# Performance work log

Measured on AMD Instinct MI355X. Metric: run time of the kernel, lower is better.

## Reference

```python
import jax, jax.numpy as jnp
import numpy as np

N = 50000
E = 800000
IN_CH, CDK, EDGE_DIM = 40, 200, 10
HID, HEADS = 64, 4
NEG_SLOPE = 0.2
SM_EPS = 1e-16
BN_EPS = 1e-5


def _glorot(key, shape):
    fan = shape[0] + shape[-1]
    return jax.random.normal(key, shape, jnp.float32) * jnp.sqrt(2.0 / fan)


def setup_inputs() -> dict:
    key = jax.random.key(0)
    ks = iter(jax.random.split(key, 40))
    inp = {
        'x': jax.random.normal(next(ks), (N, IN_CH), jnp.float32),
        'cdk_desc': jax.random.normal(next(ks), (N, CDK), jnp.float32),
        'edge_src': jax.random.randint(next(ks), (E,), 0, N, jnp.int32),
        'edge_dst': jax.random.randint(next(ks), (E,), 0, N, jnp.int32),
        'edge_attr': jax.random.normal(next(ks), (E, EDGE_DIM), jnp.float32),
    }
    dims = [(IN_CH + CDK, HEADS, HID), (HID * HEADS, HEADS, HID), (HID * HEADS, 1, HID)]
    for i, (din, h, c) in enumerate(dims):
        inp[f'W{i}'] = _glorot(next(ks), (din, h * c))
        inp[f'as{i}'] = _glorot(next(ks), (h, c))
        inp[f'ad{i}'] = _glorot(next(ks), (h, c))
        inp[f'We{i}'] = _glorot(next(ks), (EDGE_DIM, h * c))
        inp[f'ae{i}'] = _glorot(next(ks), (h, c))
        inp[f'b{i}'] = jnp.zeros((h * c,), jnp.float32)
        inp[f'g{i}'] = jnp.ones((h * c,), jnp.float32)
        inp[f'be{i}'] = jnp.zeros((h * c,), jnp.float32)
    inp['linW'] = _glorot(next(ks), (HID, 1))
    inp['linB'] = jnp.zeros((1,), jnp.float32)
    return inp


def gat_conv(x, src, dst, ea, W, a_s, a_d, We, a_e, b, heads, c):
    # PyG GATConv: shared linear for src/dst, edge features, segment softmax.
    xp = (x @ W).reshape(N, heads, c)                 # [N,H,C]
    ep = (ea @ We).reshape(-1, heads, c)              # [Etot,H,C]
    al_s = (xp * a_s).sum(-1)                         # [N,H]
    al_d = (xp * a_d).sum(-1)                         # [N,H]
    al_e = (ep * a_e).sum(-1)                         # [Etot,H]
    alpha = jax.nn.leaky_relu(al_s[src] + al_d[dst] + al_e, NEG_SLOPE)
    m = jax.ops.segment_max(alpha, dst, num_segments=N)
    ex = jnp.exp(alpha - m[dst])
    den = jax.ops.segment_sum(ex, dst, num_segments=N)
    att = ex / (den[dst] + SM_EPS)                    # [Etot,H]
    out = jax.ops.segment_sum(xp[src] * att[:, :, None], dst, num_segments=N)
    return out.reshape(N, heads * c) + b


def batch_norm(x, g, be):
    mu = x.mean(0)
    var = x.var(0)
    return g * (x - mu) * jax.lax.rsqrt(var + BN_EPS) + be


def reference(x, cdk_desc, edge_src, edge_dst, edge_attr,
              W0, as0, ad0, We0, ae0, b0, g0, be0,
              W1, as1, ad1, We1, ae1, b1, g1, be1,
              W2, as2, ad2, We2, ae2, b2, g2, be2,
              linW, linB):
    # add self-loops once (PyG default add_self_loops=True, fill_value='mean')
    loop = jnp.arange(N, dtype=edge_src.dtype)
    src = jnp.concatenate([edge_src, loop])
    dst = jnp.concatenate([edge_dst, loop])
    ea_mean = edge_attr.mean(0)
    ea = jnp.concatenate([edge_attr, jnp.broadcast_to(ea_mean, (N, EDGE_DIM))], 0)

    h = jnp.concatenate([x, cdk_desc], axis=-1)
    layers = [
        (W0, as0, ad0, We0, ae0, b0, g0, be0, HEADS),
        (W1, as1, ad1, We1, ae1, b1, g1, be1, HEADS),
        (W2, as2, ad2, We2, ae2, b2, g2, be2, 1),
    ]
    for (W, a_s, a_d, We, a_e, b, g, be, heads) in layers:
        h = gat_conv(h, src, dst, ea, W, a_s, a_d, We, a_e, b, heads, HID)
        h = batch_norm(h, g, be)
        h = jax.nn.elu(h)
        # dropout is identity in eval mode
    out = h @ linW + linB
    return jax.nn.sigmoid(out).squeeze(-1)
```

## Files before the change

### kernel.cpp

```cpp
#include <hip/hip_runtime.h>
#include <math.h>

#define NNODES 50000
#define NEDGES 800000
#define ETOT   (NNODES + NEDGES)
#define EDIM   10
#define SMEPS  1e-16f
#define BNEPS  1e-5f
#define NSLOPE 0.2f

#define SCANB  ((NNODES + 255) / 256)
#define EASUMB 256
#define BNB    256

typedef _Float16 f16;
typedef f16 f16x8 __attribute__((ext_vector_type(8)));
typedef f16 f16x4 __attribute__((ext_vector_type(4)));
typedef float f32x4 __attribute__((ext_vector_type(4)));


__global__ void k_deg(const int* __restrict__ edst, int* __restrict__ deg) {
    int e = blockIdx.x * blockDim.x + threadIdx.x;
    if (e >= ETOT) return;
    int d = (e < NEDGES) ? edst[e] : (e - NEDGES);
    atomicAdd(&deg[d], 1);
}

__global__ void k_easum(const float* __restrict__ ea, float* __restrict__ part) {
    float acc[EDIM];
#pragma unroll
    for (int d = 0; d < EDIM; ++d) acc[d] = 0.f;
    int tid = blockIdx.x * blockDim.x + threadIdx.x;
    const int np = NEDGES / 2;
    for (int p = tid; p < np; p += gridDim.x * blockDim.x) {
        const float4* q = (const float4*)&ea[(long)p * 20];
        float4 v0 = q[0], v1 = q[1], v2 = q[2], v3 = q[3], v4 = q[4];
        acc[0] += v0.x + v2.z;
        acc[1] += v0.y + v2.w;
        acc[2] += v0.z + v3.x;
        acc[3] += v0.w + v3.y;
        acc[4] += v1.x + v3.z;
        acc[5] += v1.y + v3.w;
        acc[6] += v1.z + v4.x;
        acc[7] += v1.w + v4.y;
        acc[8] += v2.x + v4.z;
        acc[9] += v2.y + v4.w;
    }
    __shared__ float sm[256];
    for (int d = 0; d < EDIM; ++d) {
        sm[threadIdx.x] = acc[d];
        __syncthreads();
        for (int s = 128; s > 0; s >>= 1) {
            if (threadIdx.x < s) sm[threadIdx.x] += sm[threadIdx.x + s];
            __syncthreads();
        }
        if (threadIdx.x == 0) part[blockIdx.x * EDIM + d] = sm[0];
        __syncthreads();
    }
}

__global__ void k_scan1(const int* __restrict__ deg, int* __restrict__ off,
                        int* __restrict__ partials) {
    __shared__ int sm[256];
    int t = threadIdx.x;
    int i = blockIdx.x * 256 + t;
    int v = (i < NNODES) ? deg[i] : 0;
    sm[t] = v;
    __syncthreads();
    int val = v;
    for (int d = 1; d < 256; d <<= 1) {
        int tv = (t >= d) ? sm[t - d] : 0;
        __syncthreads();
        val += tv;
        sm[t] = val;
        __syncthreads();
    }
    if (i < NNODES) off[i] = val - v;
    if (t == 255) partials[blockIdx.x] = val;
}

__global__ void k_scan2(int* __restrict__ partials, int* __restrict__ off) {
    __shared__ int sm[256];
    int t = threadIdx.x;
    int v = (t < SCANB) ? partials[t] : 0;
    sm[t] = v;
    __syncthreads();
    int val = v;
    for (int d = 1; d < 256; d <<= 1) {
        int tv = (t >= d) ? sm[t - d] : 0;
        __syncthreads();
        val += tv;
        sm[t] = val;
        __syncthreads();
    }
    if (t < SCANB) partials[t] = val - v;
    if (t == 255) off[NNODES] = ETOT;
}

__global__ void k_scan3(int* __restrict__ off, const int* __restrict__ partials) {
    int i = blockIdx.x * 256 + threadIdx.x;
    if (i < NNODES) off[i] += partials[blockIdx.x];
}

__global__ void k_scatter(const int* __restrict__ esrc, const int* __restrict__ edst,
                          const int* __restrict__ off, int* __restrict__ cursor,
                          int* __restrict__ csr_src, int* __restrict__ perm) {
    int e = blockIdx.x * blockDim.x + threadIdx.x;
    if (e >= ETOT) return;
    int s, d;
    if (e < NEDGES) { s = esrc[e]; d = edst[e]; }
    else            { s = d = e - NEDGES; }
    int pos  = atomicAdd(&cursor[d], 1);
    int slot = off[d] + pos;
    csr_src[slot] = s;
    perm[e] = slot;
}

__global__ void k_concat_h(const float* __restrict__ x, const float* __restrict__ cdk,
                           f16* __restrict__ out) {
    int i = blockIdx.x * blockDim.x + threadIdx.x;
    if (i >= NNODES * 256) return;
    int n = i >> 8, j = i & 255;
    float v = (j < 40) ? x[n * 40 + j] : (j < 240) ? cdk[n * 200 + (j - 40)] : 0.f;
    out[i] = (f16)v;
}

__global__ void k_wcvt_all(const float* __restrict__ W0, const float* __restrict__ W1,
                           const float* __restrict__ W2, f16* __restrict__ Wt0,
                           f16* __restrict__ Wt1, f16* __restrict__ Wt2) {
    int i = blockIdx.x * blockDim.x + threadIdx.x;
    const float* W; f16* Wt; int K, NC, j;
    if (i < 65536)       { W = W0; Wt = Wt0; K = 240; NC = 256; j = i; }
    else if (i < 131072) { W = W1; Wt = Wt1; K = 256; NC = 256; j = i - 65536; }
    else if (i < 147456) { W = W2; Wt = Wt2; K = 256; NC = 64;  j = i - 131072; }
    else return;
    int n = j >> 8, k = j & 255;
    Wt[j] = (k < K) ? (f16)W[k * NC + n] : (f16)0.f;
}

#define GM_LDS 40
__global__ __launch_bounds__(256) void k_gemm_h(const f16* __restrict__ A,
                                                const f16* __restrict__ Bt,
                                                f16* __restrict__ C,
                                                int M, int NC) {
    __shared__ f16 As[128 * GM_LDS];
    __shared__ f16 Bs[64 * GM_LDS];
    const int t    = threadIdx.x;
    const int w    = t >> 6;
    const int lane = t & 63;
    const int row0 = blockIdx.x * 128;
    const int col0 = blockIdx.y * 64;

    const int ar = t >> 1;
    const int ak = (t & 1) * 16;
    const int bn = t >> 2;
    const int bk = (t & 3) * 8;

    const int l16 = lane & 15;
    const int kg  = lane >> 4;

    f32x4 acc[2][4];
#pragma unroll
    for (int i = 0; i < 2; ++i)
#pragma unroll
        for (int j = 0; j < 4; ++j) acc[i][j] = {0.f, 0.f, 0.f, 0.f};

    for (int k0 = 0; k0 < 256; k0 += 32) {
        f16x8 av0, av1;
#pragma unroll
        for (int i = 0; i < 8; ++i) { av0[i] = (f16)0.f; av1[i] = (f16)0.f; }
        if (row0 + ar < M) {
            const f16* ap = &A[(long)(row0 + ar) * 256 + k0 + ak];
            av0 = *(const f16x8*)ap;
            av1 = *(const f16x8*)(ap + 8);
        }
        *(f16x8*)&As[ar * GM_LDS + ak]     = av0;
        *(f16x8*)&As[ar * GM_LDS + ak + 8] = av1;
        f16x8 bv = *(const f16x8*)&Bt[(long)(col0 + bn) * 256 + k0 + bk];
        *(f16x8*)&Bs[bn * GM_LDS + bk] = bv;
        __syncthreads();

        f16x8 afr[2], bfr[4];
#pragma unroll
        for (int mi = 0; mi < 2; ++mi)
            afr[mi] = *(const f16x8*)&As[(w * 32 + mi * 16 + l16) * GM_LDS + kg * 8];
#pragma unroll
        for (int ni = 0; ni < 4; ++ni)
            bfr[ni] = *(const f16x8*)&Bs[(ni * 16 + l16) * GM_LDS + kg * 8];
#pragma unroll
        for (int mi = 0; mi < 2; ++mi)
#pragma unroll
            for (int ni = 0; ni < 4; ++ni)
                acc[mi][ni] = __builtin_amdgcn_mfma_f32_16x16x32_f16(
                    afr[mi], bfr[ni], acc[mi][ni], 0, 0, 0);
        __syncthreads();
    }
#pragma unroll
    for (int mi = 0; mi < 2; ++mi)
#pragma unroll
        for (int ni = 0; ni < 4; ++ni)
#pragma unroll
            for (int j = 0; j < 4; ++j) {
                int r = row0 + w * 32 + mi * 16 + kg * 4 + j;
                if (r < M) C[(long)r * NC + col0 + ni * 16 + l16] = (f16)acc[mi][ni][j];
            }
}

template <int H>
__global__ __launch_bounds__(256) void k_attn_node(const f16* __restrict__ xp,
                                                   const float* __restrict__ a_s,
                                                   const float* __restrict__ a_d,
                                                   float* __restrict__ als,
                                                   float* __restrict__ ald) {
    int gw   = (blockIdx.x * blockDim.x + threadIdx.x) >> 6;
    int lane = threadIdx.x & 63;
    if (gw >= NNODES) return;
    if constexpr (H == 4) {
        int h = lane >> 4, c4 = (lane & 15) * 4;
        f16x4 xh = *(const f16x4*)&xp[(long)gw * 256 + lane * 4];
        float4 xv = make_float4((float)xh[0], (float)xh[1], (float)xh[2], (float)xh[3]);
        float4 ws = *(const float4*)&a_s[h * 64 + c4];
        float4 wd = *(const float4*)&a_d[h * 64 + c4];
        float ps = xv.x * ws.x + xv.y * ws.y + xv.z * ws.z + xv.w * ws.w;
        float pd = xv.x * wd.x + xv.y * wd.y + xv.z * wd.z + xv.w * wd.w;
        for (int o = 1; o < 16; o <<= 1) { ps += __shfl_xor(ps, o); pd += __shfl_xor(pd, o); }
        if ((lane & 15) == 0) { als[gw * 4 + h] = ps; ald[gw * 4 + h] = pd; }
    } else {
        float xv = (float)xp[(long)gw * 64 + lane];
        float ps = xv * a_s[lane];
        float pd = xv * a_d[lane];
        for (int o = 1; o < 64; o <<= 1) { ps += __shfl_xor(ps, o); pd += __shfl_xor(pd, o); }
        if (lane == 0) { als[gw] = ps; ald[gw] = pd; }
    }
}

__global__ void k_ve_all(const float* __restrict__ We0, const float* __restrict__ ae0,
                         const float* __restrict__ We1, const float* __restrict__ ae1,
                         const float* __restrict__ We2, const float* __restrict__ ae2,
                         const float* __restrict__ eapart,
                         float* __restrict__ VeAll, float* __restrict__ laAll) {
    int l = blockIdx.x;
    const float* We = (l == 0) ? We0 : (l == 1) ? We1 : We2;
    const float* ae = (l == 0) ? ae0 : (l == 1) ? ae1 : ae2;
    int H = (l == 2) ? 1 : 4;
    float* Ve = VeAll + l * 48;
    float* la = laAll + l * 4;
    int t = threadIdx.x;

    float ac[EDIM];
#pragma unroll
    for (int d = 0; d < EDIM; ++d) ac[d] = 0.f;
    for (int r = t; r < EASUMB; r += 64) {
#pragma unroll
        for (int d = 0; d < EDIM; ++d) ac[d] += eapart[r * EDIM + d];
    }
#pragma unroll
    for (int o = 1; o < 64; o <<= 1) {
#pragma unroll
        for (int d = 0; d < EDIM; ++d) ac[d] += __shfl_xor(ac[d], o);
    }

    if (t < EDIM * H) {
        int d = t / H, h = t % H;
        float s = 0.f;
        for (int c = 0; c < 64; ++c) s += We[d * (H * 64) + h * 64 + c] * ae[h * 64 + c];
        Ve[d * H + h] = s;
    }
    __syncthreads();
    if (t < H) {
        float s = 0.f;
        for (int d = 0; d < EDIM; ++d) s += (ac[d] * (1.0f / NEDGES)) * Ve[d * H + t];
        la[t] = s;
    }
}

template <int H>
__global__ void k_edge(const float* __restrict__ ea, const int* __restrict__ esrc,
                       const int* __restrict__ edst, const float* __restrict__ als,
                       const float* __restrict__ ald, const float* __restrict__ Ve,
                       const float* __restrict__ loop_al, const int* __restrict__ perm,
                       float* __restrict__ alpha) {
    int e = blockIdx.x * blockDim.x + threadIdx.x;
    if (e >= ETOT) return;
    int s, d;
    float ale[H];
    if (e < NEDGES) {
        s = esrc[e]; d = edst[e];
#pragma unroll
        for (int h = 0; h < H; ++h) ale[h] = 0.f;
#pragma unroll
        for (int dd = 0; dd < EDIM; ++dd) {
            float v = ea[(long)e * EDIM + dd];
#pragma unroll
            for (int h = 0; h < H; ++h) ale[h] = fmaf(v, Ve[dd * H + h], ale[h]);
        }
    } else {
        s = d = e - NEDGES;
#pragma unroll
        for (int h = 0; h < H; ++h) ale[h] = loop_al[h];
    }
    int slot = perm[e];
#pragma unroll
    for (int h = 0; h < H; ++h) {
        float a = als[s * H + h] + ald[d * H + h] + ale[h];
        a = (a > 0.f) ? a : NSLOPE * a;
        alpha[(long)slot * H + h] = a;
    }
}

template <int H>
__global__ __launch_bounds__(256) void k_agg(const f16* __restrict__ xp,
                                             const float* __restrict__ alpha,
                                             const int* __restrict__ off,
                                             const int* __restrict__ csr_src,
                                             f16* __restrict__ out) {
    int gw   = (blockIdx.x * blockDim.x + threadIdx.x) >> 6;
    int lane = threadIdx.x & 63;
    if (gw >= NNODES) return;
    int o0 = off[gw], o1 = off[gw + 1];
    int cnt = o1 - o0;

    if constexpr (H == 4) {
        constexpr int T = 4;
        int h  = lane >> 4;
        int il = lane & 15;

        float av[T];
        int   idx[T];
        float mx = -INFINITY;
#pragma unroll
        for (int t = 0; t < T; ++t) {
            int s = o0 + t * 16 + il;
            bool ok = (s < o1);
            float a = ok ? alpha[(long)s * 4 + h] : -INFINITY;
            idx[t] = ok ? csr_src[s] : 0;
            av[t] = a;
            mx = fmaxf(mx, a);
        }
        for (int s = o0 + T * 16 + il; s < o1; s += 16)
            mx = fmaxf(mx, alpha[(long)s * 4 + h]);
#pragma unroll
        for (int o = 1; o < 16; o <<= 1) mx = fmaxf(mx, __shfl_xor(mx, o));

        float den = 0.f;
#pragma unroll
        for (int t = 0; t < T; ++t) {
            float e = expf(av[t] - mx);
            av[t] = e;
            den += e;
        }
        for (int s = o0 + T * 16 + il; s < o1; s += 16)
            den += expf(alpha[(long)s * 4 + h] - mx);
#pragma unroll
        for (int o = 1; o < 16; o <<= 1) den += __shfl_xor(den, o);
        float di = 1.0f / (den + SMEPS);

        if (cnt <= T * 16) {
            int half = lane >> 5;
            int ci   = lane & 31;
            int hb   = (ci >> 3) << 4;
            float a0[8], a1[8];
#pragma unroll
            for (int k = 0; k < 8; ++k) { a0[k] = 0.f; a1[k] = 0.f; }

#pragma unroll
            for (int t = 0; t < T; ++t) {
                int base = t * 16;
                if (base >= cnt) break;
                int lim = min(16, cnt - base);
                int jj = 0;
                for (; jj + 8 <= lim; jj += 8) {
                    int m0 = jj + half, m1 = jj + 2 + half;
                    int m2 = jj + 4 + half, m3 = jj + 6 + half;
                    float w0 = __shfl(av[t], hb | m0, 64);
                    int  sn0 = __shfl(idx[t], m0, 64);
                    float w1 = __shfl(av[t], hb | m1, 64);
                    int  sn1 = __shfl(idx[t], m1, 64);
                    float w2 = __shfl(av[t], hb | m2, 64);
                    int  sn2 = __shfl(idx[t], m2, 64);
                    float w3 = __shfl(av[t], hb | m3, 64);
                    int  sn3 = __shfl(idx[t], m3, 64);
                    f16x8 x0 = *(const f16x8*)&xp[(long)sn0 * 256 + ci * 8];
                    f16x8 x1 = *(const f16x8*)&xp[(long)sn1 * 256 + ci * 8];
                    f16x8 x2 = *(const f16x8*)&xp[(long)sn2 * 256 + ci * 8];
                    f16x8 x3 = *(const f16x8*)&xp[(long)sn3 * 256 + ci * 8];
#pragma unroll
                    for (int k = 0; k < 8; ++k) {
                        a0[k] = fmaf(w0, (float)x0[k], a0[k]);
                        a1[k] = fmaf(w1, (float)x1[k], a1[k]);
                        a0[k] = fmaf(w2, (float)x2[k], a0[k]);
                        a1[k] = fmaf(w3, (float)x3[k], a1[k]);
                    }
                }
                for (; jj < lim; jj += 2) {
                    int m = jj + half;
                    float w = __shfl(av[t], hb | (m & 15), 64);
                    int  sn = __shfl(idx[t], m & 15, 64);
                    f16x8 xv = *(const f16x8*)&xp[(long)sn * 256 + ci * 8];
#pragma unroll
                    for (int k = 0; k < 8; ++k)
                        a0[k] = fmaf(w, (float)xv[k], a0[k]);
                }
            }
            float di_h = __shfl(di, (ci >> 3) << 4, 64);
            f16x8 o;
#pragma unroll
            for (int k = 0; k < 8; ++k) {
                float v = a0[k] + a1[k];
                v += __shfl_xor(v, 32);
                o[k] = (f16)(v * di_h);
            }
            if (half == 0)
                *(f16x8*)&out[(long)gw * 256 + ci * 8] = o;
        } else {
            float4 acc = make_float4(0.f, 0.f, 0.f, 0.f);
            for (int s = o0; s < o1; ++s) {
                float w  = expf(alpha[(long)s * 4 + h] - mx);
                int   sn = csr_src[s];
                f16x4 xv = *(const f16x4*)&xp[(long)sn * 256 + lane * 4];
                acc.x = fmaf(w, (float)xv[0], acc.x);
                acc.y = fmaf(w, (float)xv[1], acc.y);
                acc.z = fmaf(w, (float)xv[2], acc.z);
                acc.w = fmaf(w, (float)xv[3], acc.w);
            }
            f16x4 o4 = {(f16)(acc.x * di), (f16)(acc.y * di),
                        (f16)(acc.z * di), (f16)(acc.w * di)};
            *(f16x4*)&out[(long)gw * 256 + lane * 4] = o4;
        }
    } else {
        constexpr int T = 2;
        float av[T];
        int   idx[T];
        float mx = -INFINITY;
#pragma unroll
        for (int t = 0; t < T; ++t) {
            int s = o0 + t * 64 + lane;
            bool ok = (s < o1);
            float a = ok ? alpha[s] : -INFINITY;
            idx[t] = ok ? csr_src[s] : 0;
            av[t] = a;
            mx = fmaxf(mx, a);
        }
        for (int s = o0 + T * 64 + lane; s < o1; s += 64)
            mx = fmaxf(mx, alpha[s]);
#pragma unroll
        for (int o = 1; o < 64; o <<= 1) mx = fmaxf(mx, __shfl_xor(mx, o));

        float den = 0.f;
#pragma unroll
        for (int t = 0; t < T; ++t) {
            float e = expf(av[t] - mx);
            av[t] = e;
            den += e;
        }
        for (int s = o0 + T * 64 + lane; s < o1; s += 64)
            den += expf(alpha[s] - mx);
#pragma unroll
        for (int o = 1; o < 64; o <<= 1) den += __shfl_xor(den, o);
        float di = 1.0f / (den + SMEPS);

        float acc0 = 0.f, acc1 = 0.f;
#pragma unroll
        for (int t = 0; t < T; ++t) {
            int base = o0 + t * 64;
            if (base >= o1) break;
            int c2 = min(64, o1 - base);
            int j = 0;
            for (; j + 4 <= c2; j += 4) {
                float w0 = __shfl(av[t],  j,     64);
                int  sn0 = __shfl(idx[t], j,     64);
                float w1 = __shfl(av[t],  j + 1, 64);
                int  sn1 = __shfl(idx[t], j + 1, 64);
                float w2 = __shfl(av[t],  j + 2, 64);
                int  sn2 = __shfl(idx[t], j + 2, 64);
                float w3 = __shfl(av[t],  j + 3, 64);
                int  sn3 = __shfl(idx[t], j + 3, 64);
                float x0 = (float)xp[(long)sn0 * 64 + lane];
                float x1 = (float)xp[(long)sn1 * 64 + lane];
                float x2 = (float)xp[(long)sn2 * 64 + lane];
                float x3 = (float)xp[(long)sn3 * 64 + lane];
                acc0 = fmaf(w0, x0, acc0);
                acc1 = fmaf(w1, x1, acc1);
                acc0 = fmaf(w2, x2, acc0);
                acc1 = fmaf(w3, x3, acc1);
            }
            for (; j < c2; ++j) {
                float w  = __shfl(av[t],  j, 64);
                int   sn = __shfl(idx[t], j, 64);
                acc0 = fmaf(w, (float)xp[(long)sn * 64 + lane], acc0);
            }
        }
        for (int s = o0 + T * 64; s < o1; ++s) {
            float w  = expf(alpha[s] - mx);
            int   sn = csr_src[s];
            acc0 = fmaf(w, (float)xp[(long)sn * 64 + lane], acc0);
        }
        out[(long)gw * 64 + lane] = (f16)((acc0 + acc1) * di);
    }
}

__global__ void k_bnstats(const f16* __restrict__ x, int width,
                          float* __restrict__ s1p, float* __restrict__ s2p) {
    __shared__ float sa[256], sb[256];
    int col  = threadIdx.x % width;
    int rsub = threadIdx.x / width;
    int rpb  = 256 / width;
    float a = 0.f, b = 0.f;
    for (int r = blockIdx.x * rpb + rsub; r < NNODES; r += gridDim.x * rpb) {
        float v = (float)x[(long)r * width + col];
        a += v; b += v * v;
    }
    if (rpb == 1) {
        s1p[blockIdx.x * width + col] = a;
        s2p[blockIdx.x * width + col] = b;
    } else {
        sa[threadIdx.x] = a;
        sb[threadIdx.x] = b;
        __syncthreads();
        if (rsub == 0) {
            for (int k = 1; k < rpb; ++k) {
                a += sa[col + k * width];
                b += sb[col + k * width];
            }
            s1p[blockIdx.x * width + col] = a;
            s2p[blockIdx.x * width + col] = b;
        }
    }
}

__global__ void k_bnfin(const float* __restrict__ s1p, const float* __restrict__ s2p,
                        const float* __restrict__ g, const float* __restrict__ be,
                        int width, float* __restrict__ scale, float* __restrict__ shift) {
    int c = threadIdx.x;
    if (c >= width) return;
    float s1 = 0.f, s2 = 0.f;
    for (int k = 0; k < BNB; ++k) {
        s1 += s1p[k * width + c];
        s2 += s2p[k * width + c];
    }
    float mu  = s1 * (1.0f / NNODES);
    float var = s2 * (1.0f / NNODES) - mu * mu;
    float sc  = g[c] * rsqrtf(var + BNEPS);
    scale[c] = sc;
    shift[c] = be[c] - mu * sc;
}

__global__ void k_bnelu_h(const f16* __restrict__ xin, f16* __restrict__ xout,
                          const float* __restrict__ scale, const float* __restrict__ shift,
                          int width) {
    long i = (long)(blockIdx.x * blockDim.x + threadIdx.x);
    long total = (long)NNODES * width;
    if (i * 4 >= total) return;
    f16x4 v4 = *(const f16x4*)&xin[i * 4];
    int c = (int)((i * 4) % width);
    float4 sc = *(const float4*)&scale[c];
    float4 sh = *(const float4*)&shift[c];
    float y0 = (float)v4[0] * sc.x + sh.x;
    float y1 = (float)v4[1] * sc.y + sh.y;
    float y2 = (float)v4[2] * sc.z + sh.z;
    float y3 = (float)v4[3] * sc.w + sh.w;
    y0 = (y0 > 0.f) ? y0 : expm1f(y0);
    y1 = (y1 > 0.f) ? y1 : expm1f(y1);
    y2 = (y2 > 0.f) ? y2 : expm1f(y2);
    y3 = (y3 > 0.f) ? y3 : expm1f(y3);
    f16x4 o = {(f16)y0, (f16)y1, (f16)y2, (f16)y3};
    *(f16x4*)&xout[i * 4] = o;
}

__global__ __launch_bounds__(256) void k_final(const f16* __restrict__ h,
                                               const float* __restrict__ linW,
                                               const float* __restrict__ linB,
                                               float* __restrict__ out) {
    int gw   = (blockIdx.x * blockDim.x + threadIdx.x) >> 6;
    int lane = threadIdx.x & 63;
    if (gw >= NNODES) return;
    float v = (float)h[(long)gw * 64 + lane] * linW[lane];
    for (int o = 32; o > 0; o >>= 1) v += __shfl_xor(v, o);
    if (lane == 0) out[gw] = 1.0f / (1.0f + expf(-(v + linB[0])));
}

extern "C" void kernel_launch(void* const* d_in, const int* in_sizes, int n_in,
                              void* d_out, int out_size, void* d_ws, size_t ws_size,
                              hipStream_t stream) {
    (void)in_sizes; (void)n_in; (void)out_size; (void)ws_size;
    const float* x    = (const float*)d_in[0];
    const float* cdk  = (const float*)d_in[1];
    const int*   esrc = (const int*)d_in[2];
    const int*   edst = (const int*)d_in[3];
    const float* ea   = (const float*)d_in[4];
    const float* W[3]   = {(const float*)d_in[5],  (const float*)d_in[13], (const float*)d_in[21]};
    const float* as_[3] = {(const float*)d_in[6],  (const float*)d_in[14], (const float*)d_in[22]};
    const float* ad_[3] = {(const float*)d_in[7],  (const float*)d_in[15], (const float*)d_in[23]};
    const float* We_[3] = {(const float*)d_in[8],  (const float*)d_in[16], (const float*)d_in[24]};
    const float* ae_[3] = {(const float*)d_in[9],  (const float*)d_in[17], (const float*)d_in[25]};
    const float* g_[3]  = {(const float*)d_in[11], (const float*)d_in[19], (const float*)d_in[27]};
    const float* be_[3] = {(const float*)d_in[12], (const float*)d_in[20], (const float*)d_in[28]};
    const float* linW = (const float*)d_in[29];
    const float* linB = (const float*)d_in[30];
    float* out = (float*)d_out;

    char* base = (char*)d_ws;
    size_t p = 0;
    auto alloc = [&](size_t bytes) -> void* {
        void* r = base + p;
        p = (p + bytes + 255) & ~(size_t)255;
        return r;
    };
    int*   deg     = (int*)alloc((size_t)NNODES * 4);
    int*   cursor  = (int*)alloc((size_t)NNODES * 4);
    size_t zero_bytes = p;
    int*   off     = (int*)alloc((size_t)(NNODES + 1) * 4);
    int*   partials= (int*)alloc((size_t)SCANB * 4);
    float* eapart  = (float*)alloc((size_t)EASUMB * EDIM * 4);
    float* s1p     = (float*)alloc((size_t)BNB * 256 * 4);
    float* s2p     = (float*)alloc((size_t)BNB * 256 * 4);
    int*   csr_src = (int*)alloc((size_t)ETOT * 4);
    int*   perm    = (int*)alloc((size_t)ETOT * 4);
    float* alpha   = (float*)alloc((size_t)ETOT * 4 * 4);
    float* als     = (float*)alloc((size_t)NNODES * 4 * 4);
    float* ald     = (float*)alloc((size_t)NNODES * 4 * 4);
    float* VeAll   = (float*)alloc((size_t)3 * 48 * 4);
    float* laAll   = (float*)alloc((size_t)3 * 4 * 4);
    float* scale   = (float*)alloc(256 * 4);
    float* shift   = (float*)alloc(256 * 4);
    f16*   Wt[3];
    Wt[0]          = (f16*)alloc((size_t)256 * 256 * 2);
    Wt[1]          = (f16*)alloc((size_t)256 * 256 * 2);
    Wt[2]          = (f16*)alloc((size_t)64 * 256 * 2);
    f16*   bufA_h  = (f16*)alloc((size_t)NNODES * 256 * 2);
    f16*   bufXp_h = (f16*)alloc((size_t)NNODES * 256 * 2);
    f16*   bufC_h  = (f16*)alloc((size_t)NNODES * 256 * 2);

    hipMemsetAsync(base, 0, zero_bytes, stream);

    int eb = (ETOT + 255) / 256;
    k_deg<<<eb, 256, 0, stream>>>(edst, deg);
    k_easum<<<EASUMB, 256, 0, stream>>>(ea, eapart);
    k_scan1<<<SCANB, 256, 0, stream>>>(deg, off, partials);
    k_scan2<<<1, 256, 0, stream>>>(partials, off);
    k_scan3<<<SCANB, 256, 0, stream>>>(off, partials);
    k_scatter<<<eb, 256, 0, stream>>>(esrc, edst, off, cursor, csr_src, perm);
    k_concat_h<<<(NNODES * 256 + 255) / 256, 256, 0, stream>>>(x, cdk, bufA_h);
    k_wcvt_all<<<576, 256, 0, stream>>>(W[0], W[1], W[2], Wt[0], Wt[1], Wt[2]);
    k_ve_all<<<3, 64, 0, stream>>>(We_[0], ae_[0], We_[1], ae_[1], We_[2], ae_[2],
                                   eapart, VeAll, laAll);

    const int nodeblocks = (NNODES * 64) / 256;
    const int mblocks = (NNODES + 127) / 128;

    for (int l = 0; l < 3; ++l) {
        const int H  = (l == 2) ? 1 : 4;
        const int NC = H * 64;
        const float* Ve  = VeAll + l * 48;
        const float* la  = laAll + l * 4;
        dim3 gg(mblocks, NC / 64);
        k_gemm_h<<<gg, 256, 0, stream>>>(bufA_h, Wt[l], bufXp_h, NNODES, NC);
        if (H == 4) {
            k_attn_node<4><<<nodeblocks, 256, 0, stream>>>(bufXp_h, as_[l], ad_[l], als, ald);
            k_edge<4><<<eb, 256, 0, stream>>>(ea, esrc, edst, als, ald, Ve, la, perm, alpha);
            k_agg<4><<<nodeblocks, 256, 0, stream>>>(bufXp_h, alpha, off, csr_src, bufC_h);
        } else {
            k_attn_node<1><<<nodeblocks, 256, 0, stream>>>(bufXp_h, as_[l], ad_[l], als, ald);
            k_edge<1><<<eb, 256, 0, stream>>>(ea, esrc, edst, als, ald, Ve, la, perm, alpha);
            k_agg<1><<<nodeblocks, 256, 0, stream>>>(bufXp_h, alpha, off, csr_src, bufC_h);
        }
        k_bnstats<<<BNB, 256, 0, stream>>>(bufC_h, NC, s1p, s2p);
        k_bnfin<<<1, 256, 0, stream>>>(s1p, s2p, g_[l], be_[l], NC, scale, shift);
        k_bnelu_h<<<(NNODES * NC / 4 + 255) / 256, 256, 0, stream>>>(bufC_h, bufA_h, scale, shift, NC);
    }
    k_final<<<nodeblocks, 256, 0, stream>>>(bufA_h, linW, linB, out);
}
```

Before: 653.1 us.

## Fuse attention-score dot products into GEMM epilogue and simplify H=4 aggregation

Computes per-node source and destination attention logits directly from the fp32 MFMA accumulators in the GEMM epilogue, with a 16-lane shuffle reduction over each head's 64 columns. This removes the separate k_attn_node launches and their re-read of the projected features. The H=4 aggregation drops its two-branch path (paired half-wave f16x8 gathers for small degrees, serial loop for large) for one path: each lane gathers f16x4 per neighbour using precomputed weights, and leftover edges beyond 64 are handled serially. Logits now come from unrounded fp32 accumulators instead of fp16-stored values, so numerics shift slightly.

```diff
diff --git a/kernel.cpp b/kernel.cpp
--- a/kernel.cpp
+++ b/kernel.cpp
@@ -142,7 +142,11 @@
 __global__ __launch_bounds__(256) void k_gemm_h(const f16* __restrict__ A,
                                                 const f16* __restrict__ Bt,
                                                 f16* __restrict__ C,
-                                                int M, int NC) {
+                                                const float* __restrict__ a_s,
+                                                const float* __restrict__ a_d,
+                                                float* __restrict__ als,
+                                                float* __restrict__ ald,
+                                                int M, int NC, int H) {
     __shared__ f16 As[128 * GM_LDS];
     __shared__ f16 Bs[64 * GM_LDS];
     const int t    = threadIdx.x;
@@ -195,6 +199,7 @@
                     afr[mi], bfr[ni], acc[mi][ni], 0, 0, 0);
         __syncthreads();
     }
+
 #pragma unroll
     for (int mi = 0; mi < 2; ++mi)
 #pragma unroll
@@ -204,34 +209,33 @@
                 int r = row0 + w * 32 + mi * 16 + kg * 4 + j;
                 if (r < M) C[(long)r * NC + col0 + ni * 16 + l16] = (f16)acc[mi][ni][j];
             }
-}
-
-template <int H>
-__global__ __launch_bounds__(256) void k_attn_node(const f16* __restrict__ xp,
-                                                   const float* __restrict__ a_s,
-                                                   const float* __restrict__ a_d,
-                                                   float* __restrict__ als,
-                                                   float* __restrict__ ald) {
-    int gw   = (blockIdx.x * blockDim.x + threadIdx.x) >> 6;
-    int lane = threadIdx.x & 63;
-    if (gw >= NNODES) return;
-    if constexpr (H == 4) {
-        int h = lane >> 4, c4 = (lane & 15) * 4;
-        f16x4 xh = *(const f16x4*)&xp[(long)gw * 256 + lane * 4];
-        float4 xv = make_float4((float)xh[0], (float)xh[1], (float)xh[2], (float)xh[3]);
-        float4 ws = *(const float4*)&a_s[h * 64 + c4];
-        float4 wd = *(const float4*)&a_d[h * 64 + c4];
-        float ps = xv.x * ws.x + xv.y * ws.y + xv.z * ws.z + xv.w * ws.w;
-        float pd = xv.x * wd.x + xv.y * wd.y + xv.z * wd.z + xv.w * wd.w;
-        for (int o = 1; o < 16; o <<= 1) { ps += __shfl_xor(ps, o); pd += __shfl_xor(pd, o); }
-        if ((lane & 15) == 0) { als[gw * 4 + h] = ps; ald[gw * 4 + h] = pd; }
-    } else {
-        float xv = (float)xp[(long)gw * 64 + lane];
-        float ps = xv * a_s[lane];
-        float pd = xv * a_d[lane];
-        for (int o = 1; o < 64; o <<= 1) { ps += __shfl_xor(ps, o); pd += __shfl_xor(pd, o); }
-        if (lane == 0) { als[gw] = ps; ald[gw] = pd; }
-    }
+
+    const int hidx = blockIdx.y;
+    float asv[4], adv[4];
+#pragma unroll
+    for (int ni = 0; ni < 4; ++ni) {
+        asv[ni] = a_s[hidx * 64 + ni * 16 + l16];
+        adv[ni] = a_d[hidx * 64 + ni * 16 + l16];
+    }
+#pragma unroll
+    for (int mi = 0; mi < 2; ++mi)
+#pragma unroll
+        for (int j = 0; j < 4; ++j) {
+            float ps = acc[mi][0][j] * asv[0] + acc[mi][1][j] * asv[1]
+                     + acc[mi][2][j] * asv[2] + acc[mi][3][j] * asv[3];
+            float pd = acc[mi][0][j] * adv[0] + acc[mi][1][j] * adv[1]
+                     + acc[mi][2][j] * adv[2] + acc[mi][3][j] * adv[3];
+#pragma unroll
+            for (int o = 1; o < 16; o <<= 1) {
+                ps += __shfl_xor(ps, o);
+                pd += __shfl_xor(pd, o);
+            }
+            int r = row0 + w * 32 + mi * 16 + kg * 4 + j;
+            if (l16 == 0 && r < M) {
+                als[(long)r * H + hidx] = ps;
+                ald[(long)r * H + hidx] = pd;
+            }
+        }
 }
 
 __global__ void k_ve_all(const float* __restrict__ We0, const float* __restrict__ ae0,
@@ -318,12 +322,12 @@
     int lane = threadIdx.x & 63;
     if (gw >= NNODES) return;
     int o0 = off[gw], o1 = off[gw + 1];
-    int cnt = o1 - o0;
 
     if constexpr (H == 4) {
         constexpr int T = 4;
         int h  = lane >> 4;
         int il = lane & 15;
+        int glane = lane & 48;
 
         float av[T];
         int   idx[T];
@@ -355,78 +359,66 @@
         for (int o = 1; o < 16; o <<= 1) den += __shfl_xor(den, o);
         float di = 1.0f / (den + SMEPS);
 
-        if (cnt <= T * 16) {
-            int half = lane >> 5;
-            int ci   = lane & 31;
-            int hb   = (ci >> 3) << 4;
-            float a0[8], a1[8];
-#pragma unroll
-            for (int k = 0; k < 8; ++k) { a0[k] = 0.f; a1[k] = 0.f; }
-
-#pragma unroll
-            for (int t = 0; t < T; ++t) {
-                int base = t * 16;
-                if (base >= cnt) break;
-                int lim = min(16, cnt - base);
-                int jj = 0;
-                for (; jj + 8 <= lim; jj += 8) {
-                    int m0 = jj + half, m1 = jj + 2 + half;
-                    int m2 = jj + 4 + half, m3 = jj + 6 + half;
-                    float w0 = __shfl(av[t], hb | m0, 64);
-                    int  sn0 = __shfl(idx[t], m0, 64);
-                    float w1 = __shfl(av[t], hb | m1, 64);
-                    int  sn1 = __shfl(idx[t], m1, 64);
-                    float w2 = __shfl(av[t], hb | m2, 64);
-                    int  sn2 = __shfl(idx[t], m2, 64);
-                    float w3 = __shfl(av[t], hb | m3, 64);
-                    int  sn3 = __shfl(idx[t], m3, 64);
-                    f16x8 x0 = *(const f16x8*)&xp[(long)sn0 * 256 + ci * 8];
-                    f16x8 x1 = *(const f16x8*)&xp[(long)sn1 * 256 + ci * 8];
-                    f16x8 x2 = *(const f16x8*)&xp[(long)sn2 * 256 + ci * 8];
-                    f16x8 x3 = *(const f16x8*)&xp[(long)sn3 * 256 + ci * 8];
-#pragma unroll
-                    for (int k = 0; k < 8; ++k) {
-                        a0[k] = fmaf(w0, (float)x0[k], a0[k]);
-                        a1[k] = fmaf(w1, (float)x1[k], a1[k]);
-                        a0[k] = fmaf(w2, (float)x2[k], a0[k]);
-                        a1[k] = fmaf(w3, (float)x3[k], a1[k]);
-                    }
-                }
-                for (; jj < lim; jj += 2) {
-                    int m = jj + half;
-                    float w = __shfl(av[t], hb | (m & 15), 64);
-                    int  sn = __shfl(idx[t], m & 15, 64);
-                    f16x8 xv = *(const f16x8*)&xp[(long)sn * 256 + ci * 8];
-#pragma unroll
-                    for (int k = 0; k < 8; ++k)
-                        a0[k] = fmaf(w, (float)xv[k], a0[k]);
-                }
-            }
-            float di_h = __shfl(di, (ci >> 3) << 4, 64);
-            f16x8 o;
-#pragma unroll
-            for (int k = 0; k < 8; ++k) {
-                float v = a0[k] + a1[k];
-                v += __shfl_xor(v, 32);
-                o[k] = (f16)(v * di_h);
-            }
-            if (half == 0)
-                *(f16x8*)&out[(long)gw * 256 + ci * 8] = o;
-        } else {
-            float4 acc = make_float4(0.f, 0.f, 0.f, 0.f);
-            for (int s = o0; s < o1; ++s) {
-                float w  = expf(alpha[(long)s * 4 + h] - mx);
-                int   sn = csr_src[s];
-                f16x4 xv = *(const f16x4*)&xp[(long)sn * 256 + lane * 4];
-                acc.x = fmaf(w, (float)xv[0], acc.x);
-                acc.y = fmaf(w, (float)xv[1], acc.y);
-                acc.z = fmaf(w, (float)xv[2], acc.z);
-                acc.w = fmaf(w, (float)xv[3], acc.w);
-            }
-            f16x4 o4 = {(f16)(acc.x * di), (f16)(acc.y * di),
-                        (f16)(acc.z * di), (f16)(acc.w * di)};
-            *(f16x4*)&out[(long)gw * 256 + lane * 4] = o4;
-        }
+        float4 acc0 = make_float4(0.f, 0.f, 0.f, 0.f);
+        float4 acc1 = make_float4(0.f, 0.f, 0.f, 0.f);
+#pragma unroll
+        for (int t = 0; t < T; ++t) {
+            int base = o0 + t * 16;
+            if (base >= o1) break;
+            int cnt = min(16, o1 - base);
+            int j = 0;
+            for (; j + 4 <= cnt; j += 4) {
+                float w0 = __shfl(av[t],  glane + j,     64);
+                int  sn0 = __shfl(idx[t], glane + j,     64);
+                float w1 = __shfl(av[t],  glane + j + 1, 64);
+                int  sn1 = __shfl(idx[t], glane + j + 1, 64);
+                float w2 = __shfl(av[t],  glane + j + 2, 64);
+                int  sn2 = __shfl(idx[t], glane + j + 2, 64);
+                float w3 = __shfl(av[t],  glane + j + 3, 64);
+                int  sn3 = __shfl(idx[t], glane + j + 3, 64);
+                f16x4 x0 = *(const f16x4*)&xp[(long)sn0 * 256 + lane * 4];
+                f16x4 x1 = *(const f16x4*)&xp[(long)sn1 * 256 + lane * 4];
+                f16x4 x2 = *(const f16x4*)&xp[(long)sn2 * 256 + lane * 4];
+                f16x4 x3 = *(const f16x4*)&xp[(long)sn3 * 256 + lane * 4];
+                acc0.x = fmaf(w0, (float)x0[0], acc0.x);
+                acc0.y = fmaf(w0, (float)x0[1], acc0.y);
+                acc0.z = fmaf(w0, (float)x0[2], acc0.z);
+                acc0.w = fmaf(w0, (float)x0[3], acc0.w);
+                acc1.x = fmaf(w1, (float)x1[0], acc1.x);
+                acc1.y = fmaf(w1, (float)x1[1], acc1.y);
+                acc1.z = fmaf(w1, (float)x1[2], acc1.z);
+                acc1.w = fmaf(w1, (float)x1[3], acc1.w);
+                acc0.x = fmaf(w2, (float)x2[0], acc0.x);
+                acc0.y = fmaf(w2, (float)x2[1], acc0.y);
+                acc0.z = fmaf(w2, (float)x2[2], acc0.z);
+                acc0.w = fmaf(w2, (float)x2[3], acc0.w);
+                acc1.x = fmaf(w3, (float)x3[0], acc1.x);
+                acc1.y = fmaf(w3, (float)x3[1], acc1.y);
+                acc1.z = fmaf(w3, (float)x3[2], acc1.z);
+                acc1.w = fmaf(w3, (float)x3[3], acc1.w);
+            }
+            for (; j < cnt; ++j) {
+                float w  = __shfl(av[t],  glane + j, 64);
+                int   sn = __shfl(idx[t], glane + j, 64);
+                f16x4 xh = *(const f16x4*)&xp[(long)sn * 256 + lane * 4];
+                acc0.x = fmaf(w, (float)xh[0], acc0.x);
+                acc0.y = fmaf(w, (float)xh[1], acc0.y);
+                acc0.z = fmaf(w, (float)xh[2], acc0.z);
+                acc0.w = fmaf(w, (float)xh[3], acc0.w);
+            }
+        }
+        for (int s = o0 + T * 16; s < o1; ++s) {
+            float w  = expf(alpha[(long)s * 4 + h] - mx);
+            int   sn = csr_src[s];
+            f16x4 xh = *(const f16x4*)&xp[(long)sn * 256 + lane * 4];
+            acc0.x = fmaf(w, (float)xh[0], acc0.x);
+            acc0.y = fmaf(w, (float)xh[1], acc0.y);
+            acc0.z = fmaf(w, (float)xh[2], acc0.z);
+            acc0.w = fmaf(w, (float)xh[3], acc0.w);
+        }
+        f16x4 o4 = {(f16)((acc0.x + acc1.x) * di), (f16)((acc0.y + acc1.y) * di),
+                    (f16)((acc0.z + acc1.z) * di), (f16)((acc0.w + acc1.w) * di)};
+        *(f16x4*)&out[(long)gw * 256 + lane * 4] = o4;
     } else {
         constexpr int T = 2;
         float av[T];
@@ -654,13 +646,12 @@
         const float* Ve  = VeAll + l * 48;
         const float* la  = laAll + l * 4;
         dim3 gg(mblocks, NC / 64);
-        k_gemm_h<<<gg, 256, 0, stream>>>(bufA_h, Wt[l], bufXp_h, NNODES, NC);
+        k_gemm_h<<<gg, 256, 0, stream>>>(bufA_h, Wt[l], bufXp_h,
+                                         as_[l], ad_[l], als, ald, NNODES, NC, H);
         if (H == 4) {
-            k_attn_node<4><<<nodeblocks, 256, 0, stream>>>(bufXp_h, as_[l], ad_[l], als, ald);
             k_edge<4><<<eb, 256, 0, stream>>>(ea, esrc, edst, als, ald, Ve, la, perm, alpha);
             k_agg<4><<<nodeblocks, 256, 0, stream>>>(bufXp_h, alpha, off, csr_src, bufC_h);
         } else {
-            k_attn_node<1><<<nodeblocks, 256, 0, stream>>>(bufXp_h, as_[l], ad_[l], als, ald);
             k_edge<1><<<eb, 256, 0, stream>>>(ea, esrc, edst, als, ald, Ve, la, perm, alpha);
             k_agg<1><<<nodeblocks, 256, 0, stream>>>(bufXp_h, alpha, off, csr_src, bufC_h);
         }
```

After: 627.1 us. 4.0% less time.
